# Performance work log

Hardware: AMD Instinct MI355X
Metric: run time of the kernel (lower is better)

The kernel has to match this reference:

```python
import jax, jax.numpy as jnp
import numpy as np

# --- static configuration (matches init_kwargs) ---
NZ = 4000
DZ = 5.0
DT = 0.001
NPAD = 100
ORDER = 4
FREE_SURFACE = True
NZ_PAD = NZ + NPAD  # freeSurface=True -> pad only bottom
NUM_VELS = 128
NUM_SHOTS = 64

C4 = (DT / DZ) ** 2 / 12.0
# 5-point 4th-order Laplacian stencil (cross-correlation taps, as in torch conv1d)
KERNEL = np.array([-C4, 16.0 * C4, -30.0 * C4, 16.0 * C4, -C4], dtype=np.float32)
HALF = (len(KERNEL) - 1) // 2  # = 2, 'same' padding


def _sponge_mask():
    # wmask[-npad:] = exp(-0.0015^2 * k^2) for k = 1..npad (tmp reversed in original)
    k = np.arange(NPAD, 0, -1).astype(np.float32)
    tmp = np.exp(-(0.0015 ** 2) * k ** 2)[::-1]
    wmask = np.ones(NZ_PAD, dtype=np.float32)
    wmask[-NPAD:] = tmp
    return jnp.asarray(wmask)


def _stencil(u):
    # u: [V, S, L]; same-padded 5-tap cross-correlation along last axis
    up = jnp.pad(u, ((0, 0), (0, 0), (HALF, HALF)))
    L = u.shape[-1]
    out = KERNEL[0] * up[..., 0:L]
    for i in range(1, len(KERNEL)):
        out = out + KERNEL[i] * up[..., i:i + L]
    return out


def setup_inputs() -> dict:
    key = jax.random.key(0)
    k1, k2, k3, k4, k5, k6 = jax.random.split(key, 6)
    vel_noPad = jax.random.uniform(k1, (NUM_VELS, NZ), dtype=jnp.float32)
    wavelet = jax.random.normal(k2, (NUM_VELS,), dtype=jnp.float32)
    zs = jax.random.randint(k3, (NUM_VELS, NUM_SHOTS), 0, NZ)
    zr = jax.random.randint(k4, (NUM_VELS, NUM_SHOTS), 0, NZ)
    prev_wavefield = jax.random.normal(k5, (NUM_VELS, NUM_SHOTS, NZ_PAD), dtype=jnp.float32)
    curr_wavefield = jax.random.normal(k6, (NUM_VELS, NUM_SHOTS, NZ_PAD), dtype=jnp.float32)
    return {
        "vel_noPad": vel_noPad,
        "wavelet": wavelet,
        "zs": zs,
        "zr": zr,
        "prev_wavefield": prev_wavefield,
        "curr_wavefield": curr_wavefield,
    }


def reference(vel_noPad, wavelet, zs, zr, prev_wavefield, curr_wavefield):
    # pad velocity at bottom with edge value (freeSurface=True -> no top pad)
    vel = jnp.pad(vel_noPad, ((0, 0), (0, NPAD)), mode="edge")  # [V, NZ_PAD]
    vel2 = (vel ** 2)[:, None, :]  # [V, 1, NZ_PAD]

    u_partial = _stencil(curr_wavefield)
    u_next = u_partial * vel2 + 2.0 * curr_wavefield - prev_wavefield

    # vectorized source injection (replaces nested python scatter loop)
    rows = jnp.arange(NUM_VELS)[:, None]
    cols = jnp.arange(NUM_SHOTS)[None, :]
    u_next = u_next.at[rows, cols, zs].add(wavelet[:, None])

    # sponge absorbing boundary mask
    u_next = u_next * _sponge_mask()[None, None, :]

    # receiver readout
    yt_pred = u_next[rows, cols, zr]  # [V, S]

    regularizer = jnp.zeros((1, 1), dtype=jnp.float32)
    return (curr_wavefield, u_next, yt_pred, regularizer)
```

## Files before the change

kernel.cpp:

```cpp
#include <hip/hip_runtime.h>

#define NZ    4000
#define NPAD  100
#define NZP   4100
#define NROW  8192
#define NGRP  1025

__global__ __launch_bounds__(256) void prop1d(
    const float* __restrict__ vel,
    const float* __restrict__ wavelet,
    const int*   __restrict__ zs,
    const int*   __restrict__ zr,
    const float* __restrict__ prev,
    const float* __restrict__ curr,
    float* __restrict__ out0,
    float* __restrict__ out1,
    float* __restrict__ out2,
    float* __restrict__ out3)
{
    __shared__ float sc[NZP + 8];
    const int row = blockIdx.x;
    const int v   = row >> 6;
    const int tid = threadIdx.x;

    const float* crow = curr + (size_t)row * NZP;
    const float* prow = prev + (size_t)row * NZP;
    float* o0 = out0 + (size_t)row * NZP;
    float* o1 = out1 + (size_t)row * NZP;

    if (tid < 8) sc[(tid < 4) ? tid : (NZP + tid)] = 0.0f;

    for (int g = tid; g < NGRP; g += 256) {
        *(float4*)(&sc[4 + 4 * g]) = *(const float4*)(crow + 4 * g);
    }
    __syncthreads();

    const int   zsr = zs[row];
    const int   zrr = zr[row];
    const float wf  = wavelet[v];

    const double C4d = (0.001 / 5.0) * (0.001 / 5.0) / 12.0;
    const float c0 = (float)(-C4d);
    const float c1 = (float)(16.0 * C4d);
    const float c2 = (float)(-30.0 * C4d);

    for (int g = tid; g < NGRP; g += 256) {
        const int zb = 4 * g;
        float u0 = sc[zb + 2], u1 = sc[zb + 3], u2 = sc[zb + 4], u3 = sc[zb + 5];
        float u4 = sc[zb + 6], u5 = sc[zb + 7], u6 = sc[zb + 8], u7 = sc[zb + 9];

        float4 pv = *(const float4*)(prow + zb);

        float w0, w1, w2, w3;
        if (g < 1000) {
            float4 vv = *(const float4*)(vel + v * NZ + zb);
            w0 = vv.x * vv.x; w1 = vv.y * vv.y; w2 = vv.z * vv.z; w3 = vv.w * vv.w;
        } else {
            float a = vel[v * NZ + (NZ - 1)];
            w0 = w1 = w2 = w3 = a * a;
        }

        float l0 = c0 * (u0 + u4) + c1 * (u1 + u3) + c2 * u2;
        float l1 = c0 * (u1 + u5) + c1 * (u2 + u4) + c2 * u3;
        float l2 = c0 * (u2 + u6) + c1 * (u3 + u5) + c2 * u4;
        float l3 = c0 * (u3 + u7) + c1 * (u4 + u6) + c2 * u5;

        float n0 = l0 * w0 + 2.0f * u2 - pv.x;
        float n1 = l1 * w1 + 2.0f * u3 - pv.y;
        float n2 = l2 * w2 + 2.0f * u4 - pv.z;
        float n3 = l3 * w3 + 2.0f * u5 - pv.w;

        if (g < 1000) {
            int d = zsr - zb;
            if ((unsigned)d < 4u) {
                if      (d == 0) n0 += wf;
                else if (d == 1) n1 += wf;
                else if (d == 2) n2 += wf;
                else             n3 += wf;
            }
        } else {
            float k0 = (float)(zb - (NZ - 1));
            float k1 = k0 + 1.0f, k2 = k0 + 2.0f, k3 = k0 + 3.0f;
            n0 *= expf(-2.25e-6f * k0 * k0);
            n1 *= expf(-2.25e-6f * k1 * k1);
            n2 *= expf(-2.25e-6f * k2 * k2);
            n3 *= expf(-2.25e-6f * k3 * k3);
        }

        {
            int d = zrr - zb;
            if ((unsigned)d < 4u) {
                out2[row] = (d == 0) ? n0 : (d == 1) ? n1 : (d == 2) ? n2 : n3;
            }
        }

        float4 cs; cs.x = u2; cs.y = u3; cs.z = u4; cs.w = u5;
        *(float4*)(o0 + zb) = cs;
        float4 ns; ns.x = n0; ns.y = n1; ns.z = n2; ns.w = n3;
        *(float4*)(o1 + zb) = ns;
    }

    if (row == 0 && tid == 0) out3[0] = 0.0f;
}

extern "C" void kernel_launch(void* const* d_in, const int* in_sizes, int n_in,
                              void* d_out, int out_size, void* d_ws, size_t ws_size,
                              hipStream_t stream) {
    const float* vel     = (const float*)d_in[0];
    const float* wavelet = (const float*)d_in[1];
    const int*   zs      = (const int*)d_in[2];
    const int*   zr      = (const int*)d_in[3];
    const float* prev    = (const float*)d_in[4];
    const float* curr    = (const float*)d_in[5];

    float* out0 = (float*)d_out;
    float* out1 = out0 + (size_t)NROW * NZP;
    float* out2 = out1 + (size_t)NROW * NZP;
    float* out3 = out2 + NROW;

    prop1d<<<NROW, 256, 0, stream>>>(vel, wavelet, zs, zr, prev, curr,
                                     out0, out1, out2, out3);
}
```

Before: 451.3 us.

## Drop LDS staging, read stencil halos from global, use nontemporal loads/stores

Removes the shared-memory copy of the current wavefield row and the block barrier. Each thread now reads its float4 plus two-element halos directly from global memory, relying on cache hits for the overlapping halo reads. Prev loads and both output stores become nontemporal, and the group loop is fully unrolled into four iterations plus one tail. The trade-off is redundant halo traffic and extra small loads in exchange for removing the sync and LDS round trip in this memory-bound kernel.

```diff
diff --git a/kernel.cpp b/kernel.cpp
--- a/kernel.cpp
+++ b/kernel.cpp
@@ -5,6 +5,9 @@
 #define NZP   4100
 #define NROW  8192
 #define NGRP  1025
+
+typedef float f32x4 __attribute__((ext_vector_type(4)));
+typedef float f32x2 __attribute__((ext_vector_type(2)));
 
 __global__ __launch_bounds__(256) void prop1d(
     const float* __restrict__ vel,
@@ -18,22 +21,14 @@
     float* __restrict__ out2,
     float* __restrict__ out3)
 {
-    __shared__ float sc[NZP + 8];
     const int row = blockIdx.x;
     const int v   = row >> 6;
     const int tid = threadIdx.x;
 
-    const float* crow = curr + (size_t)row * NZP;
-    const float* prow = prev + (size_t)row * NZP;
-    float* o0 = out0 + (size_t)row * NZP;
-    float* o1 = out1 + (size_t)row * NZP;
-
-    if (tid < 8) sc[(tid < 4) ? tid : (NZP + tid)] = 0.0f;
-
-    for (int g = tid; g < NGRP; g += 256) {
-        *(float4*)(&sc[4 + 4 * g]) = *(const float4*)(crow + 4 * g);
-    }
-    __syncthreads();
+    const float* __restrict__ crow = curr + (size_t)row * NZP;
+    const float* __restrict__ prow = prev + (size_t)row * NZP;
+    float* __restrict__ o0 = out0 + (size_t)row * NZP;
+    float* __restrict__ o1 = out1 + (size_t)row * NZP;
 
     const int   zsr = zs[row];
     const int   zrr = zr[row];
@@ -44,34 +39,48 @@
     const float c1 = (float)(16.0 * C4d);
     const float c2 = (float)(-30.0 * C4d);
 
-    for (int g = tid; g < NGRP; g += 256) {
+    auto process = [&](int g) {
         const int zb = 4 * g;
-        float u0 = sc[zb + 2], u1 = sc[zb + 3], u2 = sc[zb + 4], u3 = sc[zb + 5];
-        float u4 = sc[zb + 6], u5 = sc[zb + 7], u6 = sc[zb + 8], u7 = sc[zb + 9];
 
-        float4 pv = *(const float4*)(prow + zb);
+        const f32x4 cc = *(const f32x4*)(crow + zb);
+
+        float um2, um1, up4, up5;
+        if (g != 0) {
+            const f32x2 t = *(const f32x2*)(crow + zb - 2);
+            um2 = t.x; um1 = t.y;
+        } else {
+            um2 = 0.0f; um1 = 0.0f;
+        }
+        if (g != NGRP - 1) {
+            const f32x2 t = *(const f32x2*)(crow + zb + 4);
+            up4 = t.x; up5 = t.y;
+        } else {
+            up4 = 0.0f; up5 = 0.0f;
+        }
+
+        const f32x4 pv = __builtin_nontemporal_load((const f32x4*)(prow + zb));
 
         float w0, w1, w2, w3;
         if (g < 1000) {
-            float4 vv = *(const float4*)(vel + v * NZ + zb);
+            const f32x4 vv = *(const f32x4*)(vel + v * NZ + zb);
             w0 = vv.x * vv.x; w1 = vv.y * vv.y; w2 = vv.z * vv.z; w3 = vv.w * vv.w;
         } else {
-            float a = vel[v * NZ + (NZ - 1)];
+            const float a = vel[v * NZ + (NZ - 1)];
             w0 = w1 = w2 = w3 = a * a;
         }
 
-        float l0 = c0 * (u0 + u4) + c1 * (u1 + u3) + c2 * u2;
-        float l1 = c0 * (u1 + u5) + c1 * (u2 + u4) + c2 * u3;
-        float l2 = c0 * (u2 + u6) + c1 * (u3 + u5) + c2 * u4;
-        float l3 = c0 * (u3 + u7) + c1 * (u4 + u6) + c2 * u5;
+        const float l0 = c0 * (um2 + cc.z) + c1 * (um1 + cc.y) + c2 * cc.x;
+        const float l1 = c0 * (um1 + cc.w) + c1 * (cc.x + cc.z) + c2 * cc.y;
+        const float l2 = c0 * (cc.x + up4) + c1 * (cc.y + cc.w) + c2 * cc.z;
+        const float l3 = c0 * (cc.y + up5) + c1 * (cc.z + up4) + c2 * cc.w;
 
-        float n0 = l0 * w0 + 2.0f * u2 - pv.x;
-        float n1 = l1 * w1 + 2.0f * u3 - pv.y;
-        float n2 = l2 * w2 + 2.0f * u4 - pv.z;
-        float n3 = l3 * w3 + 2.0f * u5 - pv.w;
+        float n0 = l0 * w0 + 2.0f * cc.x - pv.x;
+        float n1 = l1 * w1 + 2.0f * cc.y - pv.y;
+        float n2 = l2 * w2 + 2.0f * cc.z - pv.z;
+        float n3 = l3 * w3 + 2.0f * cc.w - pv.w;
 
         if (g < 1000) {
-            int d = zsr - zb;
+            const int d = zsr - zb;
             if ((unsigned)d < 4u) {
                 if      (d == 0) n0 += wf;
                 else if (d == 1) n1 += wf;
@@ -79,8 +88,8 @@
                 else             n3 += wf;
             }
         } else {
-            float k0 = (float)(zb - (NZ - 1));
-            float k1 = k0 + 1.0f, k2 = k0 + 2.0f, k3 = k0 + 3.0f;
+            const float k0 = (float)(zb - (NZ - 1));
+            const float k1 = k0 + 1.0f, k2 = k0 + 2.0f, k3 = k0 + 3.0f;
             n0 *= expf(-2.25e-6f * k0 * k0);
             n1 *= expf(-2.25e-6f * k1 * k1);
             n2 *= expf(-2.25e-6f * k2 * k2);
@@ -88,17 +97,20 @@
         }
 
         {
-            int d = zrr - zb;
+            const int d = zrr - zb;
             if ((unsigned)d < 4u) {
                 out2[row] = (d == 0) ? n0 : (d == 1) ? n1 : (d == 2) ? n2 : n3;
             }
         }
 
-        float4 cs; cs.x = u2; cs.y = u3; cs.z = u4; cs.w = u5;
-        *(float4*)(o0 + zb) = cs;
-        float4 ns; ns.x = n0; ns.y = n1; ns.z = n2; ns.w = n3;
-        *(float4*)(o1 + zb) = ns;
-    }
+        __builtin_nontemporal_store(cc, (f32x4*)(o0 + zb));
+        f32x4 ns; ns.x = n0; ns.y = n1; ns.z = n2; ns.w = n3;
+        __builtin_nontemporal_store(ns, (f32x4*)(o1 + zb));
+    };
+
+    #pragma unroll
+    for (int k = 0; k < 4; ++k) process(tid + (k << 8));
+    if (tid == 255) process(1024);
 
     if (row == 0 && tid == 0) out3[0] = 0.0f;
 }
```

Result: slower. 460.7 us (+2.1%).
